# Kernel optimization log

Hardware: AMD Instinct MI355X
Metric: run time of the kernel (lower is better)

The kernel has to match this reference:

```python
import jax, jax.numpy as jnp
import numpy as np

SAMPLES = 16        # samples per spatial dim -> M = SAMPLES**2 sample points
SAMPLE_PAD = 0
K = 9               # nearest neighbors == conv kernel size == stride


def setup_inputs() -> dict:
    key = jax.random.key(0)
    k1, k2, k3 = jax.random.split(key, 3)
    B, C, H, W = 16, 128, 64, 64
    OUT = 128
    x = jax.random.normal(k1, (B, C, H, W), dtype=jnp.float32)
    w = jax.random.normal(k2, (OUT, C, K), dtype=jnp.float32) * 0.05
    b = jax.random.normal(k3, (OUT,), dtype=jnp.float32) * 0.05
    return {"x": x, "w": w, "b": b}


def reference(x, w, b):
    B, C, H, W = x.shape
    N = H * W
    # --- spatial sample grid (static, shape-derived) ---
    xi = jnp.round(jnp.linspace(SAMPLE_PAD, H - SAMPLE_PAD - 1, SAMPLES)).astype(jnp.int32)
    yi = jnp.round(jnp.linspace(SAMPLE_PAD, W - SAMPLE_PAD - 1, SAMPLES)).astype(jnp.int32)
    xg, yg = jnp.meshgrid(xi, yi, indexing='ij')
    x_sample = x[:, :, xg, yg].reshape(B, C, -1)          # (B, C, M)
    x1 = x.reshape(B, C, N)                                # (B, C, N)
    # --- squared Euclidean distance between tokens and samples ---
    dots = jnp.einsum('bcn,bcm->bnm', x1, x_sample)        # (B, N, M)
    n2 = jnp.sum(x1 * x1, axis=1)                          # (B, N)
    m2 = jnp.sum(x_sample * x_sample, axis=1)              # (B, M)
    dist2 = n2[:, :, None] + m2[:, None, :] - 2.0 * dots   # (B, N, M)
    # K nearest samples per token (smallest distance)
    _, idx = jax.lax.top_k(-dist2, K)                      # (B, N, K) int32
    # gather neighbor features from the sample set: (B, C, N, K)
    nbrs = jnp.take_along_axis(x_sample[:, :, None, :],
                               idx[:, None, :, :], axis=3)
    # Conv1d(kernel=K, stride=K) over the (B, C, N*K) prime tensor
    out = jnp.einsum('bcnk,ock->bon', nbrs, w) + b[None, :, None]
    return out.reshape(B, w.shape[0], H, W)
```

## Files before the change

### kernel.cpp

```cpp
#include <hip/hip_runtime.h>

#define NB   16
#define NC   128
#define NN   4096
#define NM   256
#define NK   9
#define NO   128

#define DELTA 0.03f

typedef __attribute__((ext_vector_type(8))) short bf16x8;
typedef __attribute__((ext_vector_type(4))) float f32x4;

__device__ __constant__ int d_grid16[16] = {0,4,8,13,17,21,25,29,34,38,42,46,50,55,59,63};

__device__ inline unsigned short bf16_rne(float v) {
    unsigned u = __float_as_uint(v);
    return (unsigned short)((u + 0x7FFFu + ((u >> 16) & 1u)) >> 16);
}

__global__ __launch_bounds__(256) void k_prep(const float* __restrict__ x,
                                              const float* __restrict__ w,
                                              float* __restrict__ xsT,
                                              unsigned short* __restrict__ xsTh,
                                              unsigned short* __restrict__ xsTl,
                                              unsigned short* __restrict__ Wth,
                                              unsigned short* __restrict__ Wtl,
                                              float* __restrict__ n2g,
                                              float* __restrict__ m2) {
    __shared__ float tile[16 * 260];
    int bx = blockIdx.x, t = threadIdx.x;
    if (bx < 128) {
        int b = bx >> 3, c0 = (bx & 7) * 16;
        int m = t;
        int pix = d_grid16[m >> 4] * 64 + d_grid16[m & 15];
        #pragma unroll
        for (int cc = 0; cc < 16; ++cc)
            tile[cc * 260 + m] = x[((size_t)b * NC + c0 + cc) * NN + pix];
        __syncthreads();
        #pragma unroll
        for (int e = 0; e < 4; ++e) {
            float fv[4];
            fv[0] = tile[(4 * e + 0) * 260 + m];
            fv[1] = tile[(4 * e + 1) * 260 + m];
            fv[2] = tile[(4 * e + 2) * 260 + m];
            fv[3] = tile[(4 * e + 3) * 260 + m];
            size_t base = ((size_t)b * NM + m) * NC + c0 + 4 * e;
            *(float4*)&xsT[base] = make_float4(fv[0], fv[1], fv[2], fv[3]);
            unsigned short h4[4], l4[4];
            #pragma unroll
            for (int e2 = 0; e2 < 4; ++e2) {
                unsigned short h = bf16_rne(fv[e2]);
                h4[e2] = h;
                l4[e2] = bf16_rne(fv[e2] - __uint_as_float(((unsigned)h) << 16));
            }
            *(ushort4*)&xsTh[base] = make_ushort4(h4[0], h4[1], h4[2], h4[3]);
            *(ushort4*)&xsTl[base] = make_ushort4(l4[0], l4[1], l4[2], l4[3]);
        }
    } else if (bx < 704) {
        int f = (bx - 128) * 256 + t;
        int ko = f >> 7, c = f & 127;
        int o = ko & 127, k = ko >> 7;
        float v = w[(size_t)o * 1152 + c * 9 + k];
        unsigned short h = bf16_rne(v);
        Wth[f] = h;
        Wtl[f] = bf16_rne(v - __uint_as_float(((unsigned)h) << 16));
    } else if (bx < 960) {
        #pragma clang fp contract(off)
        int i = bx - 704;
        int b = i >> 4, n = (i & 15) * 256 + t;
        const float* p = x + (size_t)b * NC * NN + n;
        float a = 0.f;
        #pragma unroll 4
        for (int c = 0; c < NC; ++c) { float v = p[(size_t)c * NN]; a = __fadd_rn(a, __fmul_rn(v, v)); }
        n2g[(size_t)b * NN + n] = a;
    } else {
        #pragma clang fp contract(off)
        int b = bx - 960;
        int pix = d_grid16[t >> 4] * 64 + d_grid16[t & 15];
        const float* p = x + (size_t)b * NC * NN + pix;
        float a = 0.f;
        #pragma unroll 4
        for (int c = 0; c < NC; ++c) { float v = p[(size_t)c * NN]; a = __fadd_rn(a, __fmul_rn(v, v)); }
        m2[b * NM + t] = a;
    }
}

__global__ __launch_bounds__(256) void k_g(const unsigned short* __restrict__ xsTh,
                                           const unsigned short* __restrict__ xsTl,
                                           const unsigned short* __restrict__ Wth,
                                           const unsigned short* __restrict__ Wtl,
                                           float* __restrict__ G) {
    int id = blockIdx.x;
    int b = id & 15, r = id >> 4;
    int kk = r % 9, mt = r / 9;
    int t = threadIdx.x;
    int w = t >> 6, lane = t & 63;
    int lr = lane & 15, quad = lane >> 4;
    int m = b * NM + mt * 64 + w * 16 + lr;
    const unsigned short* aph = xsTh + (size_t)m * NC;
    const unsigned short* apl = xsTl + (size_t)m * NC;
    f32x4 acc[8];
    #pragma unroll
    for (int j = 0; j < 8; ++j) acc[j] = (f32x4){0.f, 0.f, 0.f, 0.f};
    #pragma unroll
    for (int kb = 0; kb < 4; ++kb) {
        int co = kb * 32 + quad * 8;
        bf16x8 Ah = *(const bf16x8*)&aph[co];
        bf16x8 Al = *(const bf16x8*)&apl[co];
        #pragma unroll
        for (int j = 0; j < 8; ++j) {
            size_t wrow = ((size_t)kk * 128 + 16 * j + lr) * NC + co;
            bf16x8 Bh = *(const bf16x8*)&Wth[wrow];
            bf16x8 Bl = *(const bf16x8*)&Wtl[wrow];
            acc[j] = __builtin_amdgcn_mfma_f32_16x16x32_bf16(Ah, Bh, acc[j], 0, 0, 0);
            acc[j] = __builtin_amdgcn_mfma_f32_16x16x32_bf16(Al, Bh, acc[j], 0, 0, 0);
            acc[j] = __builtin_amdgcn_mfma_f32_16x16x32_bf16(Ah, Bl, acc[j], 0, 0, 0);
        }
    }
    int mrow = b * NM + mt * 64 + w * 16 + quad * 4;
    #pragma unroll
    for (int j = 0; j < 8; ++j)
        #pragma unroll
        for (int r2 = 0; r2 < 4; ++r2)
            G[((size_t)(mrow + r2)) * 1152 + kk * 128 + 16 * j + lr] = acc[j][r2];
}

__global__ __launch_bounds__(256, 4) void k_selref(const float* __restrict__ x,
                                                   const unsigned short* __restrict__ xsTh,
                                                   const unsigned short* __restrict__ xsTl,
                                                   const float* __restrict__ xsT,
                                                   const float* __restrict__ m2,
                                                   const float* __restrict__ n2g,
                                                   int* __restrict__ idx) {
    #pragma clang fp contract(off)
    __shared__ __align__(16) float x1l[32 * 132];
    __shared__ __align__(16) unsigned keysl[16 * 256];
    __shared__ float m2l[256];
    __shared__ float n2l[32];
    __shared__ int cntl[32];
    __shared__ unsigned short candl[32 * 16];
    unsigned long long* pairs = (unsigned long long*)keysl;
    int b = blockIdx.x & 15, n0 = (blockIdx.x >> 4) * 32;
    int t = threadIdx.x;
    int w = t >> 6, lane = t & 63;
    int lr = lane & 15, quad = lane >> 4;
    m2l[t] = m2[b * NM + t];
    if (t < 32) { n2l[t] = n2g[(size_t)b * NN + n0 + t]; cntl[t] = 0; }
    #pragma unroll
    for (int it = 0; it < 4; ++it) {
        int f4 = it * 256 + t;
        int c = f4 >> 3, nn4 = (f4 & 7) * 4;
        float4 v = *(const float4*)&x[((size_t)b * NC + c) * NN + n0 + nn4];
        x1l[(nn4 + 0) * 132 + c] = v.x;
        x1l[(nn4 + 1) * 132 + c] = v.y;
        x1l[(nn4 + 2) * 132 + c] = v.z;
        x1l[(nn4 + 3) * 132 + c] = v.w;
    }
    __syncthreads();
    f32x4 acc[2][4];
    #pragma unroll
    for (int i = 0; i < 2; ++i)
        #pragma unroll
        for (int j = 0; j < 4; ++j) acc[i][j] = (f32x4){0.f, 0.f, 0.f, 0.f};
    for (int kb = 0; kb < 4; ++kb) {
        bf16x8 Ah[2], Al[2];
        #pragma unroll
        for (int i = 0; i < 2; ++i) {
            const float4 va = *(const float4*)&x1l[(16 * i + lr) * 132 + kb * 32 + quad * 8];
            const float4 vb = *(const float4*)&x1l[(16 * i + lr) * 132 + kb * 32 + quad * 8 + 4];
            float vf[8] = {va.x, va.y, va.z, va.w, vb.x, vb.y, vb.z, vb.w};
            unsigned short h8[8], l8[8];
            #pragma unroll
            for (int e = 0; e < 8; ++e) {
                unsigned short h = bf16_rne(vf[e]);
                h8[e] = h;
                l8[e] = bf16_rne(vf[e] - __uint_as_float(((unsigned)h) << 16));
            }
            Ah[i] = *(bf16x8*)h8;
            Al[i] = *(bf16x8*)l8;
        }
        bf16x8 bh[4], bl[4];
        #pragma unroll
        for (int j = 0; j < 4; ++j)
            bh[j] = *(const bf16x8*)&xsTh[((size_t)b * NM + 64 * w + 16 * j + lr) * NC + kb * 32 + quad * 8];
        #pragma unroll
        for (int i = 0; i < 2; ++i)
            #pragma unroll
            for (int j = 0; j < 4; ++j)
                acc[i][j] = __builtin_amdgcn_mfma_f32_16x16x32_bf16(Ah[i], bh[j], acc[i][j], 0, 0, 0);
        #pragma unroll
        for (int i = 0; i < 2; ++i)
            #pragma unroll
            for (int j = 0; j < 4; ++j)
                acc[i][j] = __builtin_amdgcn_mfma_f32_16x16x32_bf16(Al[i], bh[j], acc[i][j], 0, 0, 0);
        #pragma unroll
        for (int j = 0; j < 4; ++j)
            bl[j] = *(const bf16x8*)&xsTl[((size_t)b * NM + 64 * w + 16 * j + lr) * NC + kb * 32 + quad * 8];
        #pragma unroll
        for (int i = 0; i < 2; ++i)
            #pragma unroll
            for (int j = 0; j < 4; ++j)
                acc[i][j] = __builtin_amdgcn_mfma_f32_16x16x32_bf16(Ah[i], bl[j], acc[i][j], 0, 0, 0);
    }
    for (int h = 0; h < 2; ++h) {
        __syncthreads();
        #pragma unroll
        for (int r = 0; r < 4; ++r) {
            int tokL = 4 * quad + r;
            #pragma unroll
            for (int j = 0; j < 4; ++j) {
                int m = 64 * w + 16 * j + lr;
                float key = fmaf(-2.f, acc[h][j][r], m2l[m]);
                unsigned u = __float_as_uint(key);
                u = (u & 0x80000000u) ? ~u : (u | 0x80000000u);
                keysl[tokL * 256 + ((m + 8 * tokL) & 255)] = u;
            }
        }
        __syncthreads();
        int tokL = t >> 4, q = t & 15;
        unsigned bk[9];
        #pragma unroll
        for (int j = 0; j < 9; ++j) bk[j] = 0xFFFFFFFFu;
        #pragma unroll
        for (int s = 0; s < 16; ++s) {
            int col = (16 * s + q + 8 * tokL) & 255;
            unsigned v = keysl[tokL * 256 + col];
            #pragma unroll
            for (int j = 0; j < 9; ++j) {
                unsigned mn = min(v, bk[j]);
                v = max(v, bk[j]);
                bk[j] = mn;
            }
        }
        #pragma unroll
        for (int d = 1; d <= 8; d <<= 1) {
            unsigned pv[9];
            #pragma unroll
            for (int j = 0; j < 9; ++j) pv[j] = (unsigned)__shfl_xor((int)bk[j], d, 64);
            #pragma unroll
            for (int j = 0; j < 9; ++j) {
                unsigned v = pv[j];
                if (v >= bk[8]) break;
                #pragma unroll
                for (int jj = 0; jj < 9; ++jj) {
                    unsigned mn = min(v, bk[jj]);
                    v = max(v, bk[jj]);
                    bk[jj] = mn;
                }
            }
        }
        unsigned u9 = bk[8];
        unsigned ku = (u9 & 0x80000000u) ? (u9 & 0x7FFFFFFFu) : ~u9;
        float thf = __uint_as_float(ku) + DELTA;
        unsigned tu = __float_as_uint(thf);
        tu = (tu & 0x80000000u) ? ~tu : (tu | 0x80000000u);
        int tok = 16 * h + tokL;
        #pragma unroll
        for (int s = 0; s < 16; ++s) {
            int col = (16 * s + q + 8 * tokL) & 255;
            unsigned v = keysl[tokL * 256 + col];
            if (v <= tu) {
                int pos = atomicAdd(&cntl[tok], 1);
                if (pos < 16) candl[tok * 16 + pos] = (unsigned short)((col - 8 * tokL) & 255);
            }
        }
    }
    __syncthreads();
    if (t < 32) {
        int c = min(cntl[t], 16);
        for (int s = c; s < 16; ++s) candl[t * 16 + s] = 0xFFFFu;
    }
    __syncthreads();
    {
        int tok = t >> 3, q8 = t & 7;
        float n2 = n2l[tok];
        int mym[2];
        unsigned long long myp[2];
        #pragma unroll
        for (int s = 0; s < 2; ++s) {
            int m = candl[tok * 16 + q8 + 8 * s];
            mym[s] = m;
            unsigned long long p = ~0ull;
            if (m != 0xFFFF) {
                const float* xt = xsT + ((size_t)b * NM + m) * NC;
                float dot = 0.f;
                for (int c4 = 0; c4 < 32; ++c4) {
                    float4 xv = *(const float4*)&x1l[tok * 132 + 4 * c4];
                    float4 sv = *(const float4*)&xt[4 * c4];
                    dot = __fadd_rn(dot, __fmul_rn(xv.x, sv.x));
                    dot = __fadd_rn(dot, __fmul_rn(xv.y, sv.y));
                    dot = __fadd_rn(dot, __fmul_rn(xv.z, sv.z));
                    dot = __fadd_rn(dot, __fmul_rn(xv.w, sv.w));
                }
                float key = __fsub_rn(__fadd_rn(n2, m2l[m]), __fmul_rn(2.f, dot));
                unsigned u = __float_as_uint(key);
                u = (u & 0x80000000u) ? ~u : (u | 0x80000000u);
                p = ((unsigned long long)u << 32) | (unsigned)m;
            }
            myp[s] = p;
            pairs[tok * 17 + q8 + 8 * s] = p;
        }
        __syncthreads();
        unsigned long long pl[16];
        #pragma unroll
        for (int l2 = 0; l2 < 16; ++l2) pl[l2] = pairs[tok * 17 + l2];
        size_t obase = (size_t)(b * NN + n0 + tok) * NK;
        #pragma unroll
        for (int s = 0; s < 2; ++s) {
            if (mym[s] != 0xFFFF) {
                int rank = 0;
                #pragma unroll
                for (int l2 = 0; l2 < 16; ++l2) rank += (pl[l2] < myp[s]);
                if (rank < 9) idx[obase + rank] = mym[s];
            }
        }
    }
}

__global__ __launch_bounds__(256) void k_out(const float* __restrict__ G,
                                             const int* __restrict__ idx,
                                             const float* __restrict__ bias,
                                             float* __restrict__ out) {
    __shared__ float S[64 * 129];
    __shared__ int   idxl[576];
    __shared__ float biasl[128];
    int b = blockIdx.x & 15, n0 = (blockIdx.x >> 4) * 64;
    int t = threadIdx.x;
    if (t < 128) biasl[t] = bias[t];
    for (int f = t; f < 576; f += 256) idxl[f] = idx[(size_t)(b * NN + n0) * NK + f];
    __syncthreads();
    int o = t & 127, half = t >> 7;
    for (int p = 0; p < 32; ++p) {
        int n = p * 2 + half;
        float a = biasl[o];
        #pragma unroll
        for (int k = 0; k < 9; ++k) {
            int m = idxl[n * 9 + k];
            a += G[(((size_t)(b * NM + m)) * NK + k) * 128 + o];
        }
        S[n * 129 + o] = a;
    }
    __syncthreads();
    int nn = t & 63, ob = t >> 6;
    for (int p = 0; p < 32; ++p) {
        int o2 = p * 4 + ob;
        out[((size_t)(b * NO + o2)) * NN + n0 + nn] = S[nn * 129 + o2];
    }
}

extern "C" void kernel_launch(void* const* d_in, const int* in_sizes, int n_in,
                              void* d_out, int out_size, void* d_ws, size_t ws_size,
                              hipStream_t stream) {
    const float* x    = (const float*)d_in[0];
    const float* w    = (const float*)d_in[1];
    const float* bias = (const float*)d_in[2];
    float* out = (float*)d_out;

    float* ws   = (float*)d_ws;
    float* m2   = ws;
    float* n2g  = ws + 4096;
    float* xsT  = ws + 69632;
    float* G    = ws + 593920;
    int*   idx  = (int*)(ws + 5312512);
    unsigned short* xsTh = (unsigned short*)(ws + 5902336);
    unsigned short* xsTl = (unsigned short*)(ws + 6164480);
    unsigned short* Wth  = (unsigned short*)(ws + 6426624);
    unsigned short* Wtl  = (unsigned short*)(ws + 6500352);

    k_prep  <<<dim3(976),  dim3(256), 0, stream>>>(x, w, xsT, xsTh, xsTl, Wth, Wtl, n2g, m2);
    k_g     <<<dim3(576),  dim3(256), 0, stream>>>(xsTh, xsTl, Wth, Wtl, G);
    k_selref<<<dim3(2048), dim3(256), 0, stream>>>(x, xsTh, xsTl, xsT, m2, n2g, idx);
    k_out   <<<dim3(1024), dim3(256), 0, stream>>>(G, idx, bias, out);
}
```

Before: 224.2 us.

## Restructure kNN selection to 16 tokens per block with register sorting networks

The selection kernel now handles 16 tokens per block instead of 32 and launches twice as many blocks. The token tile is split into bf16 hi/lo parts once, in shared memory, and the MFMA roles are swapped so each lane's accumulators belong to one token. The top-9 is then found with an in-register 16-element sorting network, cross-quad shuffles and a cross-wave merge through shared memory, which drops the large shared-memory key buffer. This is meant to cut LDS traffic and barriers and raise occupancy. The cost is that the xsTh/xsTl sample loads are now repeated for twice as many blocks, and the prep kernel's norm loops are unrolled further.

Result: slower. 235.2 us (+4.9%).

```diff
diff --git a/kernel.cpp b/kernel.cpp
--- a/kernel.cpp
+++ b/kernel.cpp
@@ -71,7 +71,7 @@
         int b = i >> 4, n = (i & 15) * 256 + t;
         const float* p = x + (size_t)b * NC * NN + n;
         float a = 0.f;
-        #pragma unroll 4
+        #pragma unroll 16
         for (int c = 0; c < NC; ++c) { float v = p[(size_t)c * NN]; a = __fadd_rn(a, __fmul_rn(v, v)); }
         n2g[(size_t)b * NN + n] = a;
     } else {
@@ -80,7 +80,7 @@
         int pix = d_grid16[t >> 4] * 64 + d_grid16[t & 15];
         const float* p = x + (size_t)b * NC * NN + pix;
         float a = 0.f;
-        #pragma unroll 4
+        #pragma unroll 16
         for (int c = 0; c < NC; ++c) { float v = p[(size_t)c * NN]; a = __fadd_rn(a, __fmul_rn(v, v)); }
         m2[b * NM + t] = a;
     }
@@ -134,23 +134,28 @@
                                                    const float* __restrict__ n2g,
                                                    int* __restrict__ idx) {
     #pragma clang fp contract(off)
-    __shared__ __align__(16) float x1l[32 * 132];
-    __shared__ __align__(16) unsigned keysl[16 * 256];
+    __shared__ __align__(16) float x1l[16 * 132];
+    __shared__ __align__(16) unsigned short xhp[16 * 136];
+    __shared__ __align__(16) unsigned short xlp[16 * 136];
+    __shared__ __align__(16) unsigned wl[4 * 16 * 9];
     __shared__ float m2l[256];
-    __shared__ float n2l[32];
-    __shared__ int cntl[32];
-    __shared__ unsigned short candl[32 * 16];
-    unsigned long long* pairs = (unsigned long long*)keysl;
-    int b = blockIdx.x & 15, n0 = (blockIdx.x >> 4) * 32;
+    __shared__ float n2l[16];
+    __shared__ int cntl[16];
+    __shared__ unsigned short candl[16 * 16];
+    unsigned long long* pairs = (unsigned long long*)wl;
+
+    int b = blockIdx.x & 15, n0 = (blockIdx.x >> 4) * 16;
     int t = threadIdx.x;
     int w = t >> 6, lane = t & 63;
     int lr = lane & 15, quad = lane >> 4;
+
     m2l[t] = m2[b * NM + t];
-    if (t < 32) { n2l[t] = n2g[(size_t)b * NN + n0 + t]; cntl[t] = 0; }
-    #pragma unroll
-    for (int it = 0; it < 4; ++it) {
-        int f4 = it * 256 + t;
-        int c = f4 >> 3, nn4 = (f4 & 7) * 4;
+    if (t < 16) { n2l[t] = n2g[(size_t)b * NN + n0 + t]; cntl[t] = 0; }
+
+    #pragma unroll
+    for (int it = 0; it < 2; ++it) {
+        int f = it * 256 + t;
+        int c = f >> 2, nn4 = (f & 3) * 4;
         float4 v = *(const float4*)&x[((size_t)b * NC + c) * NN + n0 + nn4];
         x1l[(nn4 + 0) * 132 + c] = v.x;
         x1l[(nn4 + 1) * 132 + c] = v.y;
@@ -158,162 +163,167 @@
         x1l[(nn4 + 3) * 132 + c] = v.w;
     }
     __syncthreads();
-    f32x4 acc[2][4];
-    #pragma unroll
-    for (int i = 0; i < 2; ++i)
-        #pragma unroll
-        for (int j = 0; j < 4; ++j) acc[i][j] = (f32x4){0.f, 0.f, 0.f, 0.f};
+
+    {
+        int tok = t >> 4, c0 = (t & 15) * 8;
+        float vf[8];
+        *(float4*)&vf[0] = *(const float4*)&x1l[tok * 132 + c0];
+        *(float4*)&vf[4] = *(const float4*)&x1l[tok * 132 + c0 + 4];
+        unsigned short h8[8], l8[8];
+        #pragma unroll
+        for (int e = 0; e < 8; ++e) {
+            unsigned short h = bf16_rne(vf[e]);
+            h8[e] = h;
+            l8[e] = bf16_rne(vf[e] - __uint_as_float(((unsigned)h) << 16));
+        }
+        *(ushort4*)&xhp[tok * 136 + c0]     = make_ushort4(h8[0], h8[1], h8[2], h8[3]);
+        *(ushort4*)&xhp[tok * 136 + c0 + 4] = make_ushort4(h8[4], h8[5], h8[6], h8[7]);
+        *(ushort4*)&xlp[tok * 136 + c0]     = make_ushort4(l8[0], l8[1], l8[2], l8[3]);
+        *(ushort4*)&xlp[tok * 136 + c0 + 4] = make_ushort4(l8[4], l8[5], l8[6], l8[7]);
+    }
+    __syncthreads();
+
+    f32x4 acc[4];
+    #pragma unroll
+    for (int j = 0; j < 4; ++j) acc[j] = (f32x4){0.f, 0.f, 0.f, 0.f};
+    int mbase = w * 64;
+    #pragma unroll
     for (int kb = 0; kb < 4; ++kb) {
-        bf16x8 Ah[2], Al[2];
-        #pragma unroll
-        for (int i = 0; i < 2; ++i) {
-            const float4 va = *(const float4*)&x1l[(16 * i + lr) * 132 + kb * 32 + quad * 8];
-            const float4 vb = *(const float4*)&x1l[(16 * i + lr) * 132 + kb * 32 + quad * 8 + 4];
-            float vf[8] = {va.x, va.y, va.z, va.w, vb.x, vb.y, vb.z, vb.w};
-            unsigned short h8[8], l8[8];
+        bf16x8 Bh = *(const bf16x8*)&xhp[lr * 136 + kb * 32 + quad * 8];
+        bf16x8 Bl = *(const bf16x8*)&xlp[lr * 136 + kb * 32 + quad * 8];
+        #pragma unroll
+        for (int j = 0; j < 4; ++j) {
+            size_t arow = ((size_t)b * NM + mbase + 16 * j + lr) * NC + kb * 32 + quad * 8;
+            bf16x8 Ah = *(const bf16x8*)&xsTh[arow];
+            bf16x8 Al = *(const bf16x8*)&xsTl[arow];
+            acc[j] = __builtin_amdgcn_mfma_f32_16x16x32_bf16(Ah, Bh, acc[j], 0, 0, 0);
+            acc[j] = __builtin_amdgcn_mfma_f32_16x16x32_bf16(Ah, Bl, acc[j], 0, 0, 0);
+            acc[j] = __builtin_amdgcn_mfma_f32_16x16x32_bf16(Al, Bh, acc[j], 0, 0, 0);
+        }
+    }
+
+    unsigned s16[16];
+    #pragma unroll
+    for (int j = 0; j < 4; ++j)
+        #pragma unroll
+        for (int r = 0; r < 4; ++r) {
+            int m = mbase + 16 * j + quad * 4 + r;
+            float key = fmaf(-2.f, acc[j][r], m2l[m]);
+            unsigned u = __float_as_uint(key);
+            u = (u & 0x80000000u) ? ~u : (u | 0x80000000u);
+            s16[j * 4 + r] = u;
+        }
+    #define CE(i,jx) { unsigned a_ = s16[i], b_ = s16[jx]; s16[i] = min(a_, b_); s16[jx] = max(a_, b_); }
+    CE(0,1) CE(2,3) CE(0,2) CE(1,3) CE(1,2)
+    CE(4,5) CE(6,7) CE(4,6) CE(5,7) CE(5,6)
+    CE(0,4) CE(2,6) CE(2,4) CE(1,5) CE(3,7) CE(3,5) CE(1,2) CE(3,4) CE(5,6)
+    CE(8,9) CE(10,11) CE(8,10) CE(9,11) CE(9,10)
+    CE(12,13) CE(14,15) CE(12,14) CE(13,15) CE(13,14)
+    CE(8,12) CE(10,14) CE(10,12) CE(9,13) CE(11,15) CE(11,13) CE(9,10) CE(11,12) CE(13,14)
+    CE(0,8) CE(4,12) CE(4,8) CE(2,10) CE(6,14) CE(6,10) CE(2,4) CE(6,8) CE(10,12)
+    CE(1,9) CE(5,13) CE(5,9) CE(3,11) CE(7,15) CE(7,11) CE(3,5) CE(7,9) CE(11,13)
+    CE(1,2) CE(3,4) CE(5,6) CE(7,8) CE(9,10) CE(11,12) CE(13,14)
+    #undef CE
+
+    unsigned bk[9];
+    #pragma unroll
+    for (int jj = 0; jj < 9; ++jj) bk[jj] = s16[jj];
+
+    #pragma unroll
+    for (int d = 16; d <= 32; d <<= 1) {
+        unsigned pv[9];
+        #pragma unroll
+        for (int jj = 0; jj < 9; ++jj) pv[jj] = (unsigned)__shfl_xor((int)bk[jj], d, 64);
+        #pragma unroll
+        for (int jj = 0; jj < 9; ++jj) {
+            unsigned v = pv[jj];
+            if (v >= bk[8]) break;
             #pragma unroll
-            for (int e = 0; e < 8; ++e) {
-                unsigned short h = bf16_rne(vf[e]);
-                h8[e] = h;
-                l8[e] = bf16_rne(vf[e] - __uint_as_float(((unsigned)h) << 16));
-            }
-            Ah[i] = *(bf16x8*)h8;
-            Al[i] = *(bf16x8*)l8;
-        }
-        bf16x8 bh[4], bl[4];
-        #pragma unroll
-        for (int j = 0; j < 4; ++j)
-            bh[j] = *(const bf16x8*)&xsTh[((size_t)b * NM + 64 * w + 16 * j + lr) * NC + kb * 32 + quad * 8];
-        #pragma unroll
-        for (int i = 0; i < 2; ++i)
+            for (int kk = 0; kk < 9; ++kk) {
+                unsigned mn = min(v, bk[kk]);
+                v = max(v, bk[kk]);
+                bk[kk] = mn;
+            }
+        }
+    }
+
+    if (quad == 0) {
+        #pragma unroll
+        for (int jj = 0; jj < 9; ++jj) wl[(w * 16 + lr) * 9 + jj] = bk[jj];
+    }
+    __syncthreads();
+    #pragma unroll
+    for (int ww = 1; ww < 4; ++ww) {
+        int wsrc = (w + ww) & 3;
+        const unsigned* src = &wl[(wsrc * 16 + lr) * 9];
+        for (int jj = 0; jj < 9; ++jj) {
+            unsigned v = src[jj];
+            if (v >= bk[8]) break;
             #pragma unroll
-            for (int j = 0; j < 4; ++j)
-                acc[i][j] = __builtin_amdgcn_mfma_f32_16x16x32_bf16(Ah[i], bh[j], acc[i][j], 0, 0, 0);
-        #pragma unroll
-        for (int i = 0; i < 2; ++i)
-            #pragma unroll
-            for (int j = 0; j < 4; ++j)
-                acc[i][j] = __builtin_amdgcn_mfma_f32_16x16x32_bf16(Al[i], bh[j], acc[i][j], 0, 0, 0);
-        #pragma unroll
-        for (int j = 0; j < 4; ++j)
-            bl[j] = *(const bf16x8*)&xsTl[((size_t)b * NM + 64 * w + 16 * j + lr) * NC + kb * 32 + quad * 8];
-        #pragma unroll
-        for (int i = 0; i < 2; ++i)
-            #pragma unroll
-            for (int j = 0; j < 4; ++j)
-                acc[i][j] = __builtin_amdgcn_mfma_f32_16x16x32_bf16(Ah[i], bl[j], acc[i][j], 0, 0, 0);
-    }
-    for (int h = 0; h < 2; ++h) {
-        __syncthreads();
+            for (int kk = 0; kk < 9; ++kk) {
+                unsigned mn = min(v, bk[kk]);
+                v = max(v, bk[kk]);
+                bk[kk] = mn;
+            }
+        }
+    }
+
+    unsigned u9 = bk[8];
+    unsigned ku = (u9 & 0x80000000u) ? (u9 & 0x7FFFFFFFu) : ~u9;
+    float thf = __uint_as_float(ku) + DELTA;
+    unsigned tu = __float_as_uint(thf);
+    tu = (tu & 0x80000000u) ? ~tu : (tu | 0x80000000u);
+    #pragma unroll
+    for (int j = 0; j < 4; ++j)
         #pragma unroll
         for (int r = 0; r < 4; ++r) {
-            int tokL = 4 * quad + r;
-            #pragma unroll
-            for (int j = 0; j < 4; ++j) {
-                int m = 64 * w + 16 * j + lr;
-                float key = fmaf(-2.f, acc[h][j][r], m2l[m]);
-                unsigned u = __float_as_uint(key);
-                u = (u & 0x80000000u) ? ~u : (u | 0x80000000u);
-                keysl[tokL * 256 + ((m + 8 * tokL) & 255)] = u;
-            }
-        }
-        __syncthreads();
-        int tokL = t >> 4, q = t & 15;
-        unsigned bk[9];
-        #pragma unroll
-        for (int j = 0; j < 9; ++j) bk[j] = 0xFFFFFFFFu;
-        #pragma unroll
-        for (int s = 0; s < 16; ++s) {
-            int col = (16 * s + q + 8 * tokL) & 255;
-            unsigned v = keysl[tokL * 256 + col];
-            #pragma unroll
-            for (int j = 0; j < 9; ++j) {
-                unsigned mn = min(v, bk[j]);
-                v = max(v, bk[j]);
-                bk[j] = mn;
-            }
-        }
-        #pragma unroll
-        for (int d = 1; d <= 8; d <<= 1) {
-            unsigned pv[9];
-            #pragma unroll
-            for (int j = 0; j < 9; ++j) pv[j] = (unsigned)__shfl_xor((int)bk[j], d, 64);
-            #pragma unroll
-            for (int j = 0; j < 9; ++j) {
-                unsigned v = pv[j];
-                if (v >= bk[8]) break;
-                #pragma unroll
-                for (int jj = 0; jj < 9; ++jj) {
-                    unsigned mn = min(v, bk[jj]);
-                    v = max(v, bk[jj]);
-                    bk[jj] = mn;
-                }
-            }
-        }
-        unsigned u9 = bk[8];
-        unsigned ku = (u9 & 0x80000000u) ? (u9 & 0x7FFFFFFFu) : ~u9;
-        float thf = __uint_as_float(ku) + DELTA;
-        unsigned tu = __float_as_uint(thf);
-        tu = (tu & 0x80000000u) ? ~tu : (tu | 0x80000000u);
-        int tok = 16 * h + tokL;
-        #pragma unroll
-        for (int s = 0; s < 16; ++s) {
-            int col = (16 * s + q + 8 * tokL) & 255;
-            unsigned v = keysl[tokL * 256 + col];
-            if (v <= tu) {
-                int pos = atomicAdd(&cntl[tok], 1);
-                if (pos < 16) candl[tok * 16 + pos] = (unsigned short)((col - 8 * tokL) & 255);
-            }
-        }
-    }
-    __syncthreads();
-    if (t < 32) {
+            int m = mbase + 16 * j + quad * 4 + r;
+            float key = fmaf(-2.f, acc[j][r], m2l[m]);
+            unsigned u = __float_as_uint(key);
+            u = (u & 0x80000000u) ? ~u : (u | 0x80000000u);
+            if (u <= tu) {
+                int pos = atomicAdd(&cntl[lr], 1);
+                if (pos < 16) candl[lr * 16 + pos] = (unsigned short)m;
+            }
+        }
+    __syncthreads();
+    if (t < 16) {
         int c = min(cntl[t], 16);
         for (int s = c; s < 16; ++s) candl[t * 16 + s] = 0xFFFFu;
     }
     __syncthreads();
+
     {
-        int tok = t >> 3, q8 = t & 7;
+        int tok = t >> 4, q = t & 15;
         float n2 = n2l[tok];
-        int mym[2];
-        unsigned long long myp[2];
-        #pragma unroll
-        for (int s = 0; s < 2; ++s) {
-            int m = candl[tok * 16 + q8 + 8 * s];
-            mym[s] = m;
-            unsigned long long p = ~0ull;
-            if (m != 0xFFFF) {
-                const float* xt = xsT + ((size_t)b * NM + m) * NC;
-                float dot = 0.f;
-                for (int c4 = 0; c4 < 32; ++c4) {
-                    float4 xv = *(const float4*)&x1l[tok * 132 + 4 * c4];
-                    float4 sv = *(const float4*)&xt[4 * c4];
-                    dot = __fadd_rn(dot, __fmul_rn(xv.x, sv.x));
-                    dot = __fadd_rn(dot, __fmul_rn(xv.y, sv.y));
-                    dot = __fadd_rn(dot, __fmul_rn(xv.z, sv.z));
-                    dot = __fadd_rn(dot, __fmul_rn(xv.w, sv.w));
-                }
-                float key = __fsub_rn(__fadd_rn(n2, m2l[m]), __fmul_rn(2.f, dot));
-                unsigned u = __float_as_uint(key);
-                u = (u & 0x80000000u) ? ~u : (u | 0x80000000u);
-                p = ((unsigned long long)u << 32) | (unsigned)m;
-            }
-            myp[s] = p;
-            pairs[tok * 17 + q8 + 8 * s] = p;
-        }
+        int m = candl[tok * 16 + q];
+        unsigned long long p = ~0ull;
+        if (m != 0xFFFF) {
+            const float* xt = xsT + ((size_t)b * NM + m) * NC;
+            float dot = 0.f;
+            for (int c4 = 0; c4 < 32; ++c4) {
+                float4 xv = *(const float4*)&x1l[tok * 132 + 4 * c4];
+                float4 sv = *(const float4*)&xt[4 * c4];
+                dot = __fadd_rn(dot, __fmul_rn(xv.x, sv.x));
+                dot = __fadd_rn(dot, __fmul_rn(xv.y, sv.y));
+                dot = __fadd_rn(dot, __fmul_rn(xv.z, sv.z));
+                dot = __fadd_rn(dot, __fmul_rn(xv.w, sv.w));
+            }
+            float key = __fsub_rn(__fadd_rn(n2, m2l[m]), __fmul_rn(2.f, dot));
+            unsigned u = __float_as_uint(key);
+            u = (u & 0x80000000u) ? ~u : (u | 0x80000000u);
+            p = ((unsigned long long)u << 32) | (unsigned)m;
+        }
+        pairs[tok * 17 + q] = p;
         __syncthreads();
         unsigned long long pl[16];
         #pragma unroll
         for (int l2 = 0; l2 < 16; ++l2) pl[l2] = pairs[tok * 17 + l2];
-        size_t obase = (size_t)(b * NN + n0 + tok) * NK;
-        #pragma unroll
-        for (int s = 0; s < 2; ++s) {
-            if (mym[s] != 0xFFFF) {
-                int rank = 0;
-                #pragma unroll
-                for (int l2 = 0; l2 < 16; ++l2) rank += (pl[l2] < myp[s]);
-                if (rank < 9) idx[obase + rank] = mym[s];
-            }
+        if (m != 0xFFFF) {
+            int rank = 0;
+            #pragma unroll
+            for (int l2 = 0; l2 < 16; ++l2) rank += (pl[l2] < p);
+            if (rank < 9) idx[(size_t)(b * NN + n0 + tok) * NK + rank] = m;
         }
     }
 }
@@ -370,6 +380,6 @@
 
     k_prep  <<<dim3(976),  dim3(256), 0, stream>>>(x, w, xsT, xsTh, xsTl, Wth, Wtl, n2g, m2);
     k_g     <<<dim3(576),  dim3(256), 0, stream>>>(xsTh, xsTl, Wth, Wtl, G);
-    k_selref<<<dim3(2048), dim3(256), 0, stream>>>(x, xsTh, xsTl, xsT, m2, n2g, idx);
+    k_selref<<<dim3(4096), dim3(256), 0, stream>>>(x, xsTh, xsTl, xsT, m2, n2g, idx);
     k_out   <<<dim3(1024), dim3(256), 0, stream>>>(G, idx, bias, out);
 }
```

## Replace threshold candidate selection with register bitonic top-16 merge in k_selref

Applied to the files above, without the earlier changes.

The candidate-selection stage in k_selref is rewritten. Each lane packs approximate distance keys with the sample index in the low 8 bits, sorts 16 in registers with a sorting network, and merges across lanes with shuffles and across waves through a small shared buffer into an exact top-16 per token. This removes the 16x256 shared key array, the per-thread insertion sort, the delta-threshold pass and the atomic candidate counter. Token bf16 hi/lo splits are precomputed once into shared memory, the MFMA operand roles are swapped, and the prep reduction loops are unrolled further. Truncating the key's low 8 bits lowers ranking precision, which the exact fp32 rerank of 16 candidates must cover.

Result: slower. 251.7 us (+12.2%).

```diff
diff --git a/kernel.cpp b/kernel.cpp
--- a/kernel.cpp
+++ b/kernel.cpp
@@ -7,8 +7,6 @@
 #define NK   9
 #define NO   128
 
-#define DELTA 0.03f
-
 typedef __attribute__((ext_vector_type(8))) short bf16x8;
 typedef __attribute__((ext_vector_type(4))) float f32x4;
 
@@ -17,6 +15,19 @@
 __device__ inline unsigned short bf16_rne(float v) {
     unsigned u = __float_as_uint(v);
     return (unsigned short)((u + 0x7FFFu + ((u >> 16) & 1u)) >> 16);
+}
+
+__device__ inline void merge16(unsigned* s, const unsigned* q) {
+    unsigned r[16];
+    #pragma unroll
+    for (int i = 0; i < 16; ++i) r[i] = min(s[i], q[15 - i]);
+    #pragma unroll
+    for (int d = 8; d >= 1; d >>= 1)
+        #pragma unroll
+        for (int i = 0; i < 16; ++i)
+            if (!(i & d)) { unsigned a = r[i], b2 = r[i + d]; r[i] = min(a, b2); r[i + d] = max(a, b2); }
+    #pragma unroll
+    for (int i = 0; i < 16; ++i) s[i] = r[i];
 }
 
 __global__ __launch_bounds__(256) void k_prep(const float* __restrict__ x,
@@ -71,7 +82,7 @@
         int b = i >> 4, n = (i & 15) * 256 + t;
         const float* p = x + (size_t)b * NC * NN + n;
         float a = 0.f;
-        #pragma unroll 4
+        #pragma unroll 16
         for (int c = 0; c < NC; ++c) { float v = p[(size_t)c * NN]; a = __fadd_rn(a, __fmul_rn(v, v)); }
         n2g[(size_t)b * NN + n] = a;
     } else {
@@ -80,7 +91,7 @@
         int pix = d_grid16[t >> 4] * 64 + d_grid16[t & 15];
         const float* p = x + (size_t)b * NC * NN + pix;
         float a = 0.f;
-        #pragma unroll 4
+        #pragma unroll 16
         for (int c = 0; c < NC; ++c) { float v = p[(size_t)c * NN]; a = __fadd_rn(a, __fmul_rn(v, v)); }
         m2[b * NM + t] = a;
     }
@@ -135,18 +146,23 @@
                                                    int* __restrict__ idx) {
     #pragma clang fp contract(off)
     __shared__ __align__(16) float x1l[32 * 132];
-    __shared__ __align__(16) unsigned keysl[16 * 256];
+    __shared__ __align__(16) unsigned short xhp[32 * 136];
+    __shared__ __align__(16) unsigned short xlp[32 * 136];
+    __shared__ __align__(16) unsigned mrg[32 * 17 * 2];
+    __shared__ unsigned short candl[32 * 16];
     __shared__ float m2l[256];
     __shared__ float n2l[32];
-    __shared__ int cntl[32];
-    __shared__ unsigned short candl[32 * 16];
-    unsigned long long* pairs = (unsigned long long*)keysl;
+    unsigned* wl = mrg;
+    unsigned long long* pairs = (unsigned long long*)mrg;
+
     int b = blockIdx.x & 15, n0 = (blockIdx.x >> 4) * 32;
     int t = threadIdx.x;
     int w = t >> 6, lane = t & 63;
     int lr = lane & 15, quad = lane >> 4;
+
     m2l[t] = m2[b * NM + t];
-    if (t < 32) { n2l[t] = n2g[(size_t)b * NN + n0 + t]; cntl[t] = 0; }
+    if (t < 32) n2l[t] = n2g[(size_t)b * NN + n0 + t];
+
     #pragma unroll
     for (int it = 0; it < 4; ++it) {
         int f4 = it * 256 + t;
@@ -158,120 +174,115 @@
         x1l[(nn4 + 3) * 132 + c] = v.w;
     }
     __syncthreads();
+
+    {
+        int tok = t >> 3, c0 = (t & 7) * 16;
+        #pragma unroll
+        for (int g = 0; g < 4; ++g) {
+            float4 v = *(const float4*)&x1l[tok * 132 + c0 + 4 * g];
+            float vf[4] = {v.x, v.y, v.z, v.w};
+            unsigned short h4[4], l4[4];
+            #pragma unroll
+            for (int e = 0; e < 4; ++e) {
+                unsigned short h = bf16_rne(vf[e]);
+                h4[e] = h;
+                l4[e] = bf16_rne(vf[e] - __uint_as_float(((unsigned)h) << 16));
+            }
+            *(ushort4*)&xhp[tok * 136 + c0 + 4 * g] = make_ushort4(h4[0], h4[1], h4[2], h4[3]);
+            *(ushort4*)&xlp[tok * 136 + c0 + 4 * g] = make_ushort4(l4[0], l4[1], l4[2], l4[3]);
+        }
+    }
+    __syncthreads();
+
     f32x4 acc[2][4];
     #pragma unroll
     for (int i = 0; i < 2; ++i)
         #pragma unroll
         for (int j = 0; j < 4; ++j) acc[i][j] = (f32x4){0.f, 0.f, 0.f, 0.f};
+    int mbase = w * 64;
+    #pragma unroll
     for (int kb = 0; kb < 4; ++kb) {
-        bf16x8 Ah[2], Al[2];
-        #pragma unroll
-        for (int i = 0; i < 2; ++i) {
-            const float4 va = *(const float4*)&x1l[(16 * i + lr) * 132 + kb * 32 + quad * 8];
-            const float4 vb = *(const float4*)&x1l[(16 * i + lr) * 132 + kb * 32 + quad * 8 + 4];
-            float vf[8] = {va.x, va.y, va.z, va.w, vb.x, vb.y, vb.z, vb.w};
-            unsigned short h8[8], l8[8];
-            #pragma unroll
-            for (int e = 0; e < 8; ++e) {
-                unsigned short h = bf16_rne(vf[e]);
-                h8[e] = h;
-                l8[e] = bf16_rne(vf[e] - __uint_as_float(((unsigned)h) << 16));
-            }
-            Ah[i] = *(bf16x8*)h8;
-            Al[i] = *(bf16x8*)l8;
-        }
-        bf16x8 bh[4], bl[4];
+        int co = kb * 32 + quad * 8;
+        bf16x8 Bh0 = *(const bf16x8*)&xhp[lr * 136 + co];
+        bf16x8 Bl0 = *(const bf16x8*)&xlp[lr * 136 + co];
+        bf16x8 Bh1 = *(const bf16x8*)&xhp[(16 + lr) * 136 + co];
+        bf16x8 Bl1 = *(const bf16x8*)&xlp[(16 + lr) * 136 + co];
+        bf16x8 Ah[4], Al[4];
+        #pragma unroll
+        for (int j = 0; j < 4; ++j) {
+            size_t arow = ((size_t)(b * NM + mbase + 16 * j + lr)) * NC + co;
+            Ah[j] = *(const bf16x8*)&xsTh[arow];
+            Al[j] = *(const bf16x8*)&xsTl[arow];
+        }
+        #pragma unroll
+        for (int j = 0; j < 4; ++j) {
+            acc[0][j] = __builtin_amdgcn_mfma_f32_16x16x32_bf16(Ah[j], Bh0, acc[0][j], 0, 0, 0);
+            acc[0][j] = __builtin_amdgcn_mfma_f32_16x16x32_bf16(Ah[j], Bl0, acc[0][j], 0, 0, 0);
+            acc[0][j] = __builtin_amdgcn_mfma_f32_16x16x32_bf16(Al[j], Bh0, acc[0][j], 0, 0, 0);
+            acc[1][j] = __builtin_amdgcn_mfma_f32_16x16x32_bf16(Ah[j], Bh1, acc[1][j], 0, 0, 0);
+            acc[1][j] = __builtin_amdgcn_mfma_f32_16x16x32_bf16(Ah[j], Bl1, acc[1][j], 0, 0, 0);
+            acc[1][j] = __builtin_amdgcn_mfma_f32_16x16x32_bf16(Al[j], Bh1, acc[1][j], 0, 0, 0);
+        }
+    }
+
+    #pragma unroll
+    for (int h = 0; h < 2; ++h) {
+        unsigned s16v[16];
         #pragma unroll
         for (int j = 0; j < 4; ++j)
-            bh[j] = *(const bf16x8*)&xsTh[((size_t)b * NM + 64 * w + 16 * j + lr) * NC + kb * 32 + quad * 8];
-        #pragma unroll
-        for (int i = 0; i < 2; ++i)
-            #pragma unroll
-            for (int j = 0; j < 4; ++j)
-                acc[i][j] = __builtin_amdgcn_mfma_f32_16x16x32_bf16(Ah[i], bh[j], acc[i][j], 0, 0, 0);
-        #pragma unroll
-        for (int i = 0; i < 2; ++i)
-            #pragma unroll
-            for (int j = 0; j < 4; ++j)
-                acc[i][j] = __builtin_amdgcn_mfma_f32_16x16x32_bf16(Al[i], bh[j], acc[i][j], 0, 0, 0);
-        #pragma unroll
-        for (int j = 0; j < 4; ++j)
-            bl[j] = *(const bf16x8*)&xsTl[((size_t)b * NM + 64 * w + 16 * j + lr) * NC + kb * 32 + quad * 8];
-        #pragma unroll
-        for (int i = 0; i < 2; ++i)
-            #pragma unroll
-            for (int j = 0; j < 4; ++j)
-                acc[i][j] = __builtin_amdgcn_mfma_f32_16x16x32_bf16(Ah[i], bl[j], acc[i][j], 0, 0, 0);
-    }
-    for (int h = 0; h < 2; ++h) {
-        __syncthreads();
-        #pragma unroll
-        for (int r = 0; r < 4; ++r) {
-            int tokL = 4 * quad + r;
-            #pragma unroll
-            for (int j = 0; j < 4; ++j) {
-                int m = 64 * w + 16 * j + lr;
+            #pragma unroll
+            for (int r = 0; r < 4; ++r) {
+                int m = mbase + 16 * j + quad * 4 + r;
                 float key = fmaf(-2.f, acc[h][j][r], m2l[m]);
                 unsigned u = __float_as_uint(key);
                 u = (u & 0x80000000u) ? ~u : (u | 0x80000000u);
-                keysl[tokL * 256 + ((m + 8 * tokL) & 255)] = u;
+                s16v[4 * j + r] = (u & 0xFFFFFF00u) | (unsigned)m;
             }
+        #define CE(i,jx) { unsigned a_ = s16v[i], b_ = s16v[jx]; s16v[i] = min(a_, b_); s16v[jx] = max(a_, b_); }
+        CE(0,1) CE(2,3) CE(0,2) CE(1,3) CE(1,2)
+        CE(4,5) CE(6,7) CE(4,6) CE(5,7) CE(5,6)
+        CE(0,4) CE(2,6) CE(2,4) CE(1,5) CE(3,7) CE(3,5) CE(1,2) CE(3,4) CE(5,6)
+        CE(8,9) CE(10,11) CE(8,10) CE(9,11) CE(9,10)
+        CE(12,13) CE(14,15) CE(12,14) CE(13,15) CE(13,14)
+        CE(8,12) CE(10,14) CE(10,12) CE(9,13) CE(11,15) CE(11,13) CE(9,10) CE(11,12) CE(13,14)
+        CE(0,8) CE(4,12) CE(4,8) CE(2,10) CE(6,14) CE(6,10) CE(2,4) CE(6,8) CE(10,12)
+        CE(1,9) CE(5,13) CE(5,9) CE(3,11) CE(7,15) CE(7,11) CE(3,5) CE(7,9) CE(11,13)
+        CE(1,2) CE(3,4) CE(5,6) CE(7,8) CE(9,10) CE(11,12) CE(13,14)
+        #undef CE
+
+        #pragma unroll
+        for (int d = 16; d <= 32; d <<= 1) {
+            unsigned q[16];
+            #pragma unroll
+            for (int i = 0; i < 16; ++i) q[i] = (unsigned)__shfl_xor((int)s16v[i], d, 64);
+            merge16(s16v, q);
+        }
+
+        if (quad == 0) {
+            #pragma unroll
+            for (int ii = 0; ii < 4; ++ii)
+                *(uint4*)&wl[(w * 16 + lr) * 16 + 4 * ii] =
+                    make_uint4(s16v[4*ii], s16v[4*ii+1], s16v[4*ii+2], s16v[4*ii+3]);
         }
         __syncthreads();
-        int tokL = t >> 4, q = t & 15;
-        unsigned bk[9];
-        #pragma unroll
-        for (int j = 0; j < 9; ++j) bk[j] = 0xFFFFFFFFu;
-        #pragma unroll
-        for (int s = 0; s < 16; ++s) {
-            int col = (16 * s + q + 8 * tokL) & 255;
-            unsigned v = keysl[tokL * 256 + col];
-            #pragma unroll
-            for (int j = 0; j < 9; ++j) {
-                unsigned mn = min(v, bk[j]);
-                v = max(v, bk[j]);
-                bk[j] = mn;
-            }
-        }
-        #pragma unroll
-        for (int d = 1; d <= 8; d <<= 1) {
-            unsigned pv[9];
-            #pragma unroll
-            for (int j = 0; j < 9; ++j) pv[j] = (unsigned)__shfl_xor((int)bk[j], d, 64);
-            #pragma unroll
-            for (int j = 0; j < 9; ++j) {
-                unsigned v = pv[j];
-                if (v >= bk[8]) break;
-                #pragma unroll
-                for (int jj = 0; jj < 9; ++jj) {
-                    unsigned mn = min(v, bk[jj]);
-                    v = max(v, bk[jj]);
-                    bk[jj] = mn;
-                }
-            }
-        }
-        unsigned u9 = bk[8];
-        unsigned ku = (u9 & 0x80000000u) ? (u9 & 0x7FFFFFFFu) : ~u9;
-        float thf = __uint_as_float(ku) + DELTA;
-        unsigned tu = __float_as_uint(thf);
-        tu = (tu & 0x80000000u) ? ~tu : (tu | 0x80000000u);
-        int tok = 16 * h + tokL;
-        #pragma unroll
-        for (int s = 0; s < 16; ++s) {
-            int col = (16 * s + q + 8 * tokL) & 255;
-            unsigned v = keysl[tokL * 256 + col];
-            if (v <= tu) {
-                int pos = atomicAdd(&cntl[tok], 1);
-                if (pos < 16) candl[tok * 16 + pos] = (unsigned short)((col - 8 * tokL) & 255);
-            }
-        }
-    }
-    __syncthreads();
-    if (t < 32) {
-        int c = min(cntl[t], 16);
-        for (int s = c; s < 16; ++s) candl[t * 16 + s] = 0xFFFFu;
-    }
-    __syncthreads();
+        #pragma unroll
+        for (int p = 1; p < 4; ++p) {
+            int pw = (w + p) & 3;
+            unsigned q[16];
+            #pragma unroll
+            for (int i = 0; i < 16; ++i) q[i] = wl[(pw * 16 + lr) * 16 + i];
+            merge16(s16v, q);
+        }
+        if (w == 0 && quad == 0) {
+            unsigned* c32 = (unsigned*)candl;
+            #pragma unroll
+            for (int i = 0; i < 16; i += 2)
+                c32[(16 * h + lr) * 8 + (i >> 1)] =
+                    (s16v[i] & 255u) | ((s16v[i + 1] & 255u) << 16);
+        }
+        __syncthreads();
+    }
+
     {
         int tok = t >> 3, q8 = t & 7;
         float n2 = n2l[tok];
@@ -281,25 +292,21 @@
         for (int s = 0; s < 2; ++s) {
             int m = candl[tok * 16 + q8 + 8 * s];
             mym[s] = m;
-            unsigned long long p = ~0ull;
-            if (m != 0xFFFF) {
-                const float* xt = xsT + ((size_t)b * NM + m) * NC;
-                float dot = 0.f;
-                for (int c4 = 0; c4 < 32; ++c4) {
-                    float4 xv = *(const float4*)&x1l[tok * 132 + 4 * c4];
-                    float4 sv = *(const float4*)&xt[4 * c4];
-                    dot = __fadd_rn(dot, __fmul_rn(xv.x, sv.x));
-                    dot = __fadd_rn(dot, __fmul_rn(xv.y, sv.y));
-                    dot = __fadd_rn(dot, __fmul_rn(xv.z, sv.z));
-                    dot = __fadd_rn(dot, __fmul_rn(xv.w, sv.w));
-                }
-                float key = __fsub_rn(__fadd_rn(n2, m2l[m]), __fmul_rn(2.f, dot));
-                unsigned u = __float_as_uint(key);
-                u = (u & 0x80000000u) ? ~u : (u | 0x80000000u);
-                p = ((unsigned long long)u << 32) | (unsigned)m;
+            const float* xt = xsT + ((size_t)(b * NM + m)) * NC;
+            float dot = 0.f;
+            for (int c4 = 0; c4 < 32; ++c4) {
+                float4 xv = *(const float4*)&x1l[tok * 132 + 4 * c4];
+                float4 sv = *(const float4*)&xt[4 * c4];
+                dot = __fadd_rn(dot, __fmul_rn(xv.x, sv.x));
+                dot = __fadd_rn(dot, __fmul_rn(xv.y, sv.y));
+                dot = __fadd_rn(dot, __fmul_rn(xv.z, sv.z));
+                dot = __fadd_rn(dot, __fmul_rn(xv.w, sv.w));
             }
-            myp[s] = p;
-            pairs[tok * 17 + q8 + 8 * s] = p;
+            float key = __fsub_rn(__fadd_rn(n2, m2l[m]), __fmul_rn(2.f, dot));
+            unsigned u = __float_as_uint(key);
+            u = (u & 0x80000000u) ? ~u : (u | 0x80000000u);
+            myp[s] = ((unsigned long long)u << 32) | (unsigned)m;
+            pairs[tok * 17 + q8 + 8 * s] = myp[s];
         }
         __syncthreads();
         unsigned long long pl[16];
@@ -308,12 +315,10 @@
         size_t obase = (size_t)(b * NN + n0 + tok) * NK;
         #pragma unroll
         for (int s = 0; s < 2; ++s) {
-            if (mym[s] != 0xFFFF) {
-                int rank = 0;
-                #pragma unroll
-                for (int l2 = 0; l2 < 16; ++l2) rank += (pl[l2] < myp[s]);
-                if (rank < 9) idx[obase + rank] = mym[s];
-            }
+            int rank = 0;
+            #pragma unroll
+            for (int l2 = 0; l2 < 16; ++l2) rank += (pl[l2] < myp[s]);
+            if (rank < 9) idx[obase + rank] = mym[s];
         }
     }
 }
```
